# Optimization experiments

Measured on AMD Instinct MI355X. Metric: run time of the kernel, lower is better.

Reference implementation:

```python
import jax, jax.numpy as jnp
import numpy as np

LATENT = 64  # latent_size -> N = K = LATENT**2 = 4096 codes/tokens


def setup_inputs() -> dict:
    key = jax.random.key(0)
    k1, k2 = jax.random.split(key)
    hidden, L = 1024, LATENT
    z = jax.random.normal(k1, (hidden, L, L), dtype=jnp.float32)
    code_books = jax.random.uniform(k2, (hidden, L, L), dtype=jnp.float32)  # torch.rand init
    return {"z": z, "code_books": code_books}


def reference(z, code_books):
    # z, code_books: (D=hidden, L, L). Tokens/codes are columns of the flattened maps.
    D = z.shape[0]
    zf = z.reshape(D, -1).T           # (N, D) tokens
    cb = code_books.reshape(D, -1).T  # (K, D) codebook entries
    # Squared L2 distance via GEMM trick: ||a-b||^2 = ||a||^2 + ||b||^2 - 2 a.b
    # (avoids the N x K x D broadcast intermediate of the original)
    d2 = (jnp.sum(zf * zf, axis=1)[:, None]
          + jnp.sum(cb * cb, axis=1)[None, :]
          - 2.0 * zf @ cb.T)          # (N, K)
    idx = jnp.argmin(d2, axis=1)      # (N,)
    zq = cb[idx]                      # (N, D) gather
    zq = zq.reshape(LATENT, LATENT, -1).transpose(2, 0, 1)  # (D, L, L)
    # Straight-through: z = zq + (z - zq).detach()  (z was detached before lookup)
    z_st = zq + jax.lax.stop_gradient(z - zq)
    return z_st, zq
```

## Files before the change

### kernel.cpp

```cpp
#include <hip/hip_runtime.h>
#include <stdint.h>

#define D  1024
#define NK 4096
#define KA 1024
#define KB 1024
#define TAU 0.15f
#define CW  0.12f
#define MAXC 1024

#define BK2 32
#define NT2 (KA / BK2)
#define NBUF 3

typedef __attribute__((ext_vector_type(8))) _Float16 f16x8;
typedef __attribute__((ext_vector_type(4))) float f32x4;
typedef unsigned long long u64;

__device__ __forceinline__ uint32_t fkey(float f) {
    uint32_t b = __float_as_uint(f);
    return (b & 0x80000000u) ? ~b : (b | 0x80000000u);
}
__device__ __forceinline__ float unfkey(uint32_t u) {
    uint32_t b = (u & 0x80000000u) ? (u & 0x7fffffffu) : ~u;
    return __uint_as_float(b);
}
__device__ __forceinline__ u64 umin64(u64 a, u64 b) { return a < b ? a : b; }
__device__ __forceinline__ u64 umax64(u64 a, u64 b) { return a > b ? a : b; }

__device__ __forceinline__ void gload16(void* lds, const void* g) {
    __builtin_amdgcn_global_load_lds(
        (const __attribute__((address_space(1))) unsigned int*)g,
        (__attribute__((address_space(3))) unsigned int*)lds, 16, 0, 0);
}

#define BAR()      __builtin_amdgcn_s_barrier()
#define VMCNT6()   asm volatile("s_waitcnt vmcnt(6)" ::: "memory")
#define VMCNT0()   asm volatile("s_waitcnt vmcnt(0)" ::: "memory")

__global__ void cbnorm_kernel(const float* __restrict__ cb, float* __restrict__ cbn) {
    __shared__ float red[256];
    const int kk = threadIdx.x & 63;
    const int dc = threadIdx.x >> 6;
    const int k  = blockIdx.x * 64 + kk;
    float s = 0.f;
    for (int d = dc; d < D; d += 4) {
        float v = cb[d * NK + k];
        s = fmaf(v, v, s);
    }
    red[threadIdx.x] = s;
    __syncthreads();
    if (dc == 0) cbn[k] = (red[kk] + red[64 + kk]) + (red[128 + kk] + red[192 + kk]);
}

__global__ __launch_bounds__(256) void split_transpose(
        const float* __restrict__ z, const float* __restrict__ cb,
        _Float16* __restrict__ Ap, _Float16* __restrict__ Bp,
        float* __restrict__ partial) {
    __shared__ float T[64][65];
    const int isZ = (blockIdx.z == 0);
    const float* src = isZ ? z : cb;
    _Float16* dst = isZ ? Ap : Bp;
    const int n0 = blockIdx.x * 64, d0 = blockIdx.y * 64;
    const int t = threadIdx.x;
#pragma unroll
    for (int i = 0; i < 4; ++i) {
        int dl = (t >> 4) + i * 16;
        int nl = (t & 15) * 4;
        float4 v = *(const float4*)&src[(size_t)(d0 + dl) * NK + n0 + nl];
        T[dl][nl] = v.x; T[dl][nl + 1] = v.y; T[dl][nl + 2] = v.z; T[dl][nl + 3] = v.w;
    }
    __syncthreads();
    const int nr = t >> 2, dch = (t & 3) * 16;
    f16x8 h0, h1;
    float s = 0.f;
#pragma unroll
    for (int j = 0; j < 8; ++j) {
        float v = T[dch + j][nr];
        s = fmaf(v, v, s);
        h0[j] = (_Float16)v;
    }
#pragma unroll
    for (int j = 0; j < 8; ++j) {
        float v = T[dch + 8 + j][nr];
        s = fmaf(v, v, s);
        h1[j] = (_Float16)v;
    }
    size_t base = (size_t)(n0 + nr) * KA + d0 + dch;
    *(f16x8*)&dst[base]     = h0;
    *(f16x8*)&dst[base + 8] = h1;
    if (!isZ) {
        s += __shfl_xor(s, 1);
        s += __shfl_xor(s, 2);
        if ((t & 3) == 0) partial[(size_t)(d0 >> 6) * NK + n0 + nr] = s;
    }
}

__global__ void cbnorm_finish(const float* __restrict__ partial, float* __restrict__ cbn) {
    const int k = blockIdx.x * 256 + threadIdx.x;
    float s = 0.f;
#pragma unroll
    for (int j = 0; j < 16; ++j) s += partial[(size_t)j * NK + k];
    cbn[k] = s;
}

__global__ __launch_bounds__(256, 2) void gemm_mfma(
        const _Float16* __restrict__ Ap, const _Float16* __restrict__ Bp,
        const float* __restrict__ cbn, ulonglong2* __restrict__ tp) {
    __shared__ _Float16 As[NBUF][256 * BK2];
    __shared__ _Float16 Bs[NBUF][128 * BK2];
    const int tid = threadIdx.x;
    const int xcd = blockIdx.x & 7, idx = blockIdx.x >> 3;
    const int n0 = ((xcd >> 2) * 8 + (idx >> 3)) * 256;
    const int k0 = ((xcd & 3) * 8 + (idx & 7)) * 128;
    const int w = tid >> 6, l = tid & 63;
    const int wr = w >> 1, wc = w & 1;
    const int fr = l & 15, fq = l >> 4;

    f32x4 acc[8][4] = {};

    const int srow = tid >> 2;
    const int swz = ((tid & 3) ^ ((tid >> 3) & 3)) * 8;
    const _Float16* gA = Ap + (size_t)(n0 + srow) * KA + swz;
    const _Float16* gB = Bp + (size_t)(k0 + srow) * KB + swz;
    const int rcol = (fq ^ ((fr >> 1) & 3)) * 8;

#pragma unroll
    for (int i = 0; i < 4; ++i) gload16(&As[0][tid * 8 + i * 2048], gA + (size_t)(64 * i) * KA);
#pragma unroll
    for (int i = 0; i < 2; ++i) gload16(&Bs[0][tid * 8 + i * 2048], gB + (size_t)(64 * i) * KB);
#pragma unroll
    for (int i = 0; i < 4; ++i) gload16(&As[1][tid * 8 + i * 2048], gA + (size_t)(64 * i) * KA + BK2);
#pragma unroll
    for (int i = 0; i < 2; ++i) gload16(&Bs[1][tid * 8 + i * 2048], gB + (size_t)(64 * i) * KB + BK2);
    VMCNT6();
    BAR();

    int b = 0, pb = 2;
    for (int t = 0; t < NT2; ++t) {
        const _Float16* Ab = As[b];
        const _Float16* Bb = Bs[b];
        const bool st = (t + 2) < NT2;
        const size_t kofs = (size_t)(t + 2) * BK2;

        f16x8 bbf[4], a0[4], a1[4];
#pragma unroll
        for (int ni = 0; ni < 4; ++ni)
            bbf[ni] = *(const f16x8*)&Bb[(wc * 64 + ni * 16 + fr) * BK2 + rcol];
#pragma unroll
        for (int mi = 0; mi < 4; ++mi)
            a0[mi] = *(const f16x8*)&Ab[(wr * 128 + mi * 16 + fr) * BK2 + rcol];
#pragma unroll
        for (int mi = 0; mi < 4; ++mi)
            a1[mi] = *(const f16x8*)&Ab[(wr * 128 + 64 + mi * 16 + fr) * BK2 + rcol];

        if (st) {
#pragma unroll
            for (int i = 0; i < 4; ++i)
                gload16(&As[pb][tid * 8 + i * 2048], gA + (size_t)(64 * i) * KA + kofs);
#pragma unroll
            for (int i = 0; i < 2; ++i)
                gload16(&Bs[pb][tid * 8 + i * 2048], gB + (size_t)(64 * i) * KB + kofs);
        }

        __builtin_amdgcn_s_setprio(1);
#pragma unroll
        for (int mi = 0; mi < 4; ++mi)
#pragma unroll
            for (int ni = 0; ni < 4; ++ni)
                acc[mi][ni] = __builtin_amdgcn_mfma_f32_16x16x32_f16(a0[mi], bbf[ni], acc[mi][ni], 0, 0, 0);
#pragma unroll
        for (int mi = 0; mi < 4; ++mi)
#pragma unroll
            for (int ni = 0; ni < 4; ++ni)
                acc[4 + mi][ni] = __builtin_amdgcn_mfma_f32_16x16x32_f16(a1[mi], bbf[ni], acc[4 + mi][ni], 0, 0, 0);
        __builtin_amdgcn_s_setprio(0);

        if (t < NT2 - 2) {
            VMCNT6();
        } else if (t == NT2 - 2) {
            VMCNT0();
        }
        if (t < NT2 - 1) BAR();
        b = (b == 2) ? 0 : b + 1;
        pb = (pb == 2) ? 0 : pb + 1;
    }

    float cbv[4];
#pragma unroll
    for (int ni = 0; ni < 4; ++ni) cbv[ni] = cbn[k0 + wc * 64 + ni * 16 + fr];
    const int kt64 = (k0 >> 6) + wc;
#pragma unroll
    for (int mi = 0; mi < 8; ++mi) {
#pragma unroll
        for (int reg = 0; reg < 4; ++reg) {
            float b1f = 1e30f, b2f = 1e30f;
            int b1k = 0;
#pragma unroll
            for (int ni = 0; ni < 4; ++ni) {
                float s = fmaf(-2.f, acc[mi][ni][reg], cbv[ni]);
                b2f = fminf(fmaxf(s, b1f), b2f);
                if (s < b1f) { b1f = s; b1k = k0 + wc * 64 + ni * 16 + fr; }
            }
#pragma unroll
            for (int m = 8; m >= 1; m >>= 1) {
                float q1 = __shfl_xor(b1f, m);
                int   qk = __shfl_xor(b1k, m);
                float q2 = __shfl_xor(b2f, m);
                b2f = fminf(fminf(b2f, q2), fmaxf(b1f, q1));
                if (q1 < b1f) { b1f = q1; b1k = qk; }
            }
            if (fr == 0) {
                int n = n0 + wr * 128 + mi * 16 + fq * 4 + reg;
                ulonglong2 v;
                v.x = ((u64)fkey(b1f) << 32) | (unsigned)b1k;
                v.y = ((u64)fkey(b2f) << 32) | 0xffffffffu;
                tp[(size_t)kt64 * NK + n] = v;
            }
        }
    }
}

__global__ __launch_bounds__(256) void reduce_rows(
        const ulonglong2* __restrict__ tp, int* __restrict__ idx,
        int* __restrict__ rescue, u64* __restrict__ rbest, int* __restrict__ ctr) {
    __shared__ ulonglong2 sh[4][64];
    const int no = threadIdx.x & 63, st = threadIdx.x >> 6;
    const int n = blockIdx.x * 64 + no;
    u64 b1 = ~0ull, b2 = ~0ull;
#pragma unroll 4
    for (int g = st * 16; g < st * 16 + 16; ++g) {
        ulonglong2 e = tp[(size_t)g * NK + n];
        u64 nb1 = umin64(b1, e.x);
        u64 nb2 = umin64(umax64(b1, e.x), umin64(b2, e.y));
        b1 = nb1; b2 = nb2;
    }
    ulonglong2 v; v.x = b1; v.y = b2;
    sh[st][no] = v;
    __syncthreads();
    if (st == 0) {
#pragma unroll
        for (int j = 1; j < 4; ++j) {
            ulonglong2 e = sh[j][no];
            u64 nb1 = umin64(b1, e.x);
            u64 nb2 = umin64(umax64(b1, e.x), umin64(b2, e.y));
            b1 = nb1; b2 = nb2;
        }
        idx[n] = (int)(b1 & 0xffffffffull);
        float f1 = unfkey((uint32_t)(b1 >> 32));
        float f2 = unfkey((uint32_t)(b2 >> 32));
        if (f2 - f1 < TAU) {
            int p = atomicAdd(ctr, 1);
            rescue[p] = n;
            rbest[p] = ~0ull;
        }
    }
}

__global__ __launch_bounds__(256) void rescue_kernel(
        const float* __restrict__ z, const float* __restrict__ cb,
        const float* __restrict__ cbn, const ulonglong2* __restrict__ tp,
        const int* __restrict__ rescue, const int* __restrict__ ctr,
        u64* __restrict__ rbest) {
    const int cnt = min(*ctr, NK);
    const int slot = blockIdx.x;
    if (slot >= cnt) return;
    const int n = rescue[slot];
    const int tid = threadIdx.x;
    const int lane = tid & 63, wv = tid >> 6;

    __shared__ float zn[D];
    __shared__ int cand[MAXC];
    __shared__ int ccnt, overflow;
    __shared__ u64 wred[4];

    if (tid == 0) { ccnt = 0; overflow = 0; }
    for (int d = tid; d < D; d += 256) zn[d] = z[(size_t)d * NK + n];

    if (tid < 64) {
        ulonglong2 e = tp[(size_t)tid * NK + n];
        u64 m = e.x;
#pragma unroll
        for (int msk = 32; msk >= 1; msk >>= 1) m = umin64(m, __shfl_xor(m, msk));
        const float thr = unfkey((uint32_t)(m >> 32)) + CW;
        if (unfkey((uint32_t)(e.y >> 32)) < thr) {
            int p = atomicAdd(&ccnt, 64);
            if (p + 64 <= MAXC) {
                for (int j = 0; j < 64; ++j) cand[p + j] = tid * 64 + j;
            } else overflow = 1;
        } else if (unfkey((uint32_t)(e.x >> 32)) < thr) {
            int p = atomicAdd(&ccnt, 1);
            if (p < MAXC) cand[p] = (int)(e.x & 0xffffffffull);
            else overflow = 1;
        }
    }
    __syncthreads();

    const int ovf = overflow;
    const int m = ovf ? NK : min(ccnt, MAXC);
    u64 best = ~0ull;
    for (int ci = wv; ci < m; ci += 4) {
        const int k = ovf ? ci : cand[ci];
        float s = 0.f;
#pragma unroll
        for (int j = 0; j < 16; ++j)
            s = fmaf(zn[lane + j * 64], cb[(size_t)(lane + j * 64) * NK + k], s);
#pragma unroll
        for (int msk = 32; msk >= 1; msk >>= 1) s += __shfl_xor(s, msk);
        float sc = cbn[k] - 2.f * s;
        best = umin64(best, ((u64)fkey(sc) << 32) | (unsigned)k);
    }
    if (lane == 0) wred[wv] = best;
    __syncthreads();
    if (tid == 0)
        rbest[slot] = umin64(umin64(wred[0], wred[1]), umin64(wred[2], wred[3]));
}

__global__ void fix_idx(const int* __restrict__ rescue, const int* __restrict__ ctr,
                        const u64* __restrict__ rbest, int* __restrict__ idx) {
    const int cnt = min(*ctr, NK);
    for (int s = threadIdx.x + blockIdx.x * 256; s < cnt; s += gridDim.x * 256)
        idx[rescue[s]] = (int)(rbest[s] & 0xffffffffull);
}

__global__ __launch_bounds__(256) void gemm_argmin(
        const float* __restrict__ z, const float* __restrict__ cb,
        const float* __restrict__ cbn, unsigned long long* __restrict__ best) {
    __shared__ float Zs[8][128];
    __shared__ float Cs[8][128];
    const int n0 = blockIdx.y * 128, k0 = blockIdx.x * 128;
    const int tid = threadIdx.x;
    const int tx = tid & 15, ty = tid >> 4;
    const int lr = tid >> 5, lc = (tid & 31) << 2;
    float acc[8][8];
#pragma unroll
    for (int i = 0; i < 8; ++i)
#pragma unroll
        for (int j = 0; j < 8; ++j) acc[i][j] = 0.f;
    for (int d0 = 0; d0 < D; d0 += 8) {
        float4 zv = *(const float4*)&z [(d0 + lr) * NK + n0 + lc];
        float4 cv = *(const float4*)&cb[(d0 + lr) * NK + k0 + lc];
        __syncthreads();
        *(float4*)&Zs[lr][lc] = zv;
        *(float4*)&Cs[lr][lc] = cv;
        __syncthreads();
#pragma unroll
        for (int dd = 0; dd < 8; ++dd) {
            float4 a0 = *(const float4*)&Zs[dd][ty * 8];
            float4 a1 = *(const float4*)&Zs[dd][ty * 8 + 4];
            float4 b0 = *(const float4*)&Cs[dd][tx * 8];
            float4 b1 = *(const float4*)&Cs[dd][tx * 8 + 4];
            float a[8] = {a0.x, a0.y, a0.z, a0.w, a1.x, a1.y, a1.z, a1.w};
            float b[8] = {b0.x, b0.y, b0.z, b0.w, b1.x, b1.y, b1.z, b1.w};
#pragma unroll
            for (int i = 0; i < 8; ++i)
#pragma unroll
                for (int j = 0; j < 8; ++j) acc[i][j] = fmaf(a[i], b[j], acc[i][j]);
        }
    }
    float cbnv[8];
#pragma unroll
    for (int j = 0; j < 8; ++j) cbnv[j] = cbn[k0 + tx * 8 + j];
#pragma unroll
    for (int i = 0; i < 8; ++i) {
        float bv = cbnv[0] - 2.f * acc[i][0];
        int bj = 0;
#pragma unroll
        for (int j = 1; j < 8; ++j) {
            float v = cbnv[j] - 2.f * acc[i][j];
            if (v < bv) { bv = v; bj = j; }
        }
        u64 p = ((u64)fkey(bv) << 32) | (unsigned)(k0 + tx * 8 + bj);
#pragma unroll
        for (int m = 8; m >= 1; m >>= 1) {
            u64 q = __shfl_xor(p, m);
            if (q < p) p = q;
        }
        if (tx == 0) atomicMin(&best[n0 + ty * 8 + i], p);
    }
}

__global__ void extract_idx(const unsigned long long* __restrict__ best,
                            int* __restrict__ idx) {
    int n = blockIdx.x * 256 + threadIdx.x;
    idx[n] = (int)(unsigned)(best[n] & 0xFFFFFFFFull);
}

__global__ void gather_kernel(const float* __restrict__ z, const float* __restrict__ cb,
                              const int* __restrict__ idx, float* __restrict__ out) {
    const int d = blockIdx.x;
    const float* cbrow = &cb[(size_t)d * NK];
    const float* zrow  = &z [(size_t)d * NK];
    float* st = &out[(size_t)d * NK];
    float* zq = &out[(size_t)D * NK + (size_t)d * NK];
    for (int n4 = threadIdx.x; n4 < NK / 4; n4 += 256) {
        int4 iv = *(const int4*)&idx[n4 * 4];
        float4 zv = *(const float4*)&zrow[n4 * 4];
        float4 q;
        q.x = cbrow[iv.x]; q.y = cbrow[iv.y]; q.z = cbrow[iv.z]; q.w = cbrow[iv.w];
        float4 stv;
        stv.x = q.x + (zv.x - q.x);
        stv.y = q.y + (zv.y - q.y);
        stv.z = q.z + (zv.z - q.z);
        stv.w = q.w + (zv.w - q.w);
        *(float4*)&st[n4 * 4] = stv;
        *(float4*)&zq[n4 * 4] = q;
    }
}

extern "C" void kernel_launch(void* const* d_in, const int* in_sizes, int n_in,
                              void* d_out, int out_size, void* d_ws, size_t ws_size,
                              hipStream_t stream) {
    const float* z  = (const float*)d_in[0];
    const float* cb = (const float*)d_in[1];
    float* out = (float*)d_out;
    char* ws = (char*)d_ws;

    const size_t oA  = 0;
    const size_t oB  = oA + (size_t)NK * KA * 2;
    const size_t oT  = oB + (size_t)NK * KB * 2;
    const size_t oC  = oT + (size_t)NK * 64 * 16;
    const size_t oI  = oC + NK * 4;
    const size_t oR  = oI + NK * 4;
    const size_t oRB = oR + NK * 4;
    const size_t oN  = oRB + NK * 8;
    const size_t oP  = oN + 256;
    const size_t REQ = oP + (size_t)16 * NK * 4;

    if (ws_size >= REQ) {
        _Float16* Ap = (_Float16*)(ws + oA);
        _Float16* Bp = (_Float16*)(ws + oB);
        ulonglong2* tp = (ulonglong2*)(ws + oT);
        float* cbn = (float*)(ws + oC);
        int* idx = (int*)(ws + oI);
        int* rescue = (int*)(ws + oR);
        u64* rbest = (u64*)(ws + oRB);
        int* ctr = (int*)(ws + oN);
        float* partial = (float*)(ws + oP);

        hipMemsetAsync(ctr, 0, 4, stream);
        split_transpose<<<dim3(NK / 64, D / 64, 2), 256, 0, stream>>>(z, cb, Ap, Bp, partial);
        cbnorm_finish<<<16, 256, 0, stream>>>(partial, cbn);
        gemm_mfma<<<512, 256, 0, stream>>>(Ap, Bp, cbn, tp);
        reduce_rows<<<64, 256, 0, stream>>>(tp, idx, rescue, rbest, ctr);
        rescue_kernel<<<4096, 256, 0, stream>>>(z, cb, cbn, tp, rescue, ctr, rbest);
        fix_idx<<<4, 256, 0, stream>>>(rescue, ctr, rbest, idx);
        gather_kernel<<<1024, 256, 0, stream>>>(z, cb, idx, out);
    } else {
        unsigned long long* best = (unsigned long long*)ws;
        float* cbn = (float*)(ws + NK * 8);
        int* idx = (int*)(ws + NK * 8 + NK * 4);
        hipMemsetAsync(best, 0xFF, NK * 8, stream);
        cbnorm_kernel<<<64, 256, 0, stream>>>(cb, cbn);
        gemm_argmin<<<dim3(NK / 128, NK / 128), 256, 0, stream>>>(z, cb, cbn, best);
        extract_idx<<<16, 256, 0, stream>>>(best, idx);
        gather_kernel<<<1024, 256, 0, stream>>>(z, cb, idx, out);
    }
}
```

Baseline: 90.67 us.

## Load GEMM A fragments directly from global into registers, dropping A LDS staging

The A operand of the fp16 MFMA GEMM is no longer staged through LDS via triple-buffered global_load_lds. Each lane now reads its own 16-byte A fragment straight from global memory every K-step, and only B keeps the LDS pipeline. The vmcnt waits shrink to match, and a scheduling barrier is added. This removes the LDS traffic and footprint for A, which may let more blocks fit, but each wave now issues uncoalesced-ish global loads with no prefetch distance, so MFMAs may stall on global latency.

```diff
diff --git a/kernel.cpp b/kernel.cpp
--- a/kernel.cpp
+++ b/kernel.cpp
@@ -35,7 +35,8 @@
 }
 
 #define BAR()      __builtin_amdgcn_s_barrier()
-#define VMCNT6()   asm volatile("s_waitcnt vmcnt(6)" ::: "memory")
+#define SCHEDBAR() __builtin_amdgcn_sched_barrier(0)
+#define VMCNT2()   asm volatile("s_waitcnt vmcnt(2)" ::: "memory")
 #define VMCNT0()   asm volatile("s_waitcnt vmcnt(0)" ::: "memory")
 
 __global__ void cbnorm_kernel(const float* __restrict__ cb, float* __restrict__ cbn) {
@@ -107,7 +108,6 @@
 __global__ __launch_bounds__(256, 2) void gemm_mfma(
         const _Float16* __restrict__ Ap, const _Float16* __restrict__ Bp,
         const float* __restrict__ cbn, ulonglong2* __restrict__ tp) {
-    __shared__ _Float16 As[NBUF][256 * BK2];
     __shared__ _Float16 Bs[NBUF][128 * BK2];
     const int tid = threadIdx.x;
     const int xcd = blockIdx.x & 7, idx = blockIdx.x >> 3;
@@ -121,63 +121,59 @@
 
     const int srow = tid >> 2;
     const int swz = ((tid & 3) ^ ((tid >> 3) & 3)) * 8;
-    const _Float16* gA = Ap + (size_t)(n0 + srow) * KA + swz;
     const _Float16* gB = Bp + (size_t)(k0 + srow) * KB + swz;
     const int rcol = (fq ^ ((fr >> 1) & 3)) * 8;
 
-#pragma unroll
-    for (int i = 0; i < 4; ++i) gload16(&As[0][tid * 8 + i * 2048], gA + (size_t)(64 * i) * KA);
+    const _Float16* gA[8];
+#pragma unroll
+    for (int m = 0; m < 8; ++m)
+        gA[m] = Ap + (size_t)(n0 + wr * 128 + (m >> 2) * 64 + (m & 3) * 16 + fr) * KA + fq * 8;
+
 #pragma unroll
     for (int i = 0; i < 2; ++i) gload16(&Bs[0][tid * 8 + i * 2048], gB + (size_t)(64 * i) * KB);
 #pragma unroll
-    for (int i = 0; i < 4; ++i) gload16(&As[1][tid * 8 + i * 2048], gA + (size_t)(64 * i) * KA + BK2);
-#pragma unroll
     for (int i = 0; i < 2; ++i) gload16(&Bs[1][tid * 8 + i * 2048], gB + (size_t)(64 * i) * KB + BK2);
-    VMCNT6();
+    VMCNT2();
     BAR();
 
     int b = 0, pb = 2;
     for (int t = 0; t < NT2; ++t) {
-        const _Float16* Ab = As[b];
         const _Float16* Bb = Bs[b];
         const bool st = (t + 2) < NT2;
         const size_t kofs = (size_t)(t + 2) * BK2;
 
-        f16x8 bbf[4], a0[4], a1[4];
+        f16x8 av[8];
+#pragma unroll
+        for (int m = 0; m < 8; ++m)
+            av[m] = *(const f16x8*)(gA[m] + (size_t)t * BK2);
+
+        if (st) {
+#pragma unroll
+            for (int i = 0; i < 2; ++i)
+                gload16(&Bs[pb][tid * 8 + i * 2048], gB + (size_t)(64 * i) * KB + kofs);
+        }
+
+        f16x8 bbf[4];
 #pragma unroll
         for (int ni = 0; ni < 4; ++ni)
             bbf[ni] = *(const f16x8*)&Bb[(wc * 64 + ni * 16 + fr) * BK2 + rcol];
+
+        __builtin_amdgcn_s_setprio(1);
 #pragma unroll
         for (int mi = 0; mi < 4; ++mi)
-            a0[mi] = *(const f16x8*)&Ab[(wr * 128 + mi * 16 + fr) * BK2 + rcol];
+#pragma unroll
+            for (int ni = 0; ni < 4; ++ni)
+                acc[mi][ni] = __builtin_amdgcn_mfma_f32_16x16x32_f16(av[mi], bbf[ni], acc[mi][ni], 0, 0, 0);
 #pragma unroll
         for (int mi = 0; mi < 4; ++mi)
-            a1[mi] = *(const f16x8*)&Ab[(wr * 128 + 64 + mi * 16 + fr) * BK2 + rcol];
-
-        if (st) {
-#pragma unroll
-            for (int i = 0; i < 4; ++i)
-                gload16(&As[pb][tid * 8 + i * 2048], gA + (size_t)(64 * i) * KA + kofs);
-#pragma unroll
-            for (int i = 0; i < 2; ++i)
-                gload16(&Bs[pb][tid * 8 + i * 2048], gB + (size_t)(64 * i) * KB + kofs);
-        }
-
-        __builtin_amdgcn_s_setprio(1);
-#pragma unroll
-        for (int mi = 0; mi < 4; ++mi)
 #pragma unroll
             for (int ni = 0; ni < 4; ++ni)
-                acc[mi][ni] = __builtin_amdgcn_mfma_f32_16x16x32_f16(a0[mi], bbf[ni], acc[mi][ni], 0, 0, 0);
-#pragma unroll
-        for (int mi = 0; mi < 4; ++mi)
-#pragma unroll
-            for (int ni = 0; ni < 4; ++ni)
-                acc[4 + mi][ni] = __builtin_amdgcn_mfma_f32_16x16x32_f16(a1[mi], bbf[ni], acc[4 + mi][ni], 0, 0, 0);
+                acc[4 + mi][ni] = __builtin_amdgcn_mfma_f32_16x16x32_f16(av[4 + mi], bbf[ni], acc[4 + mi][ni], 0, 0, 0);
         __builtin_amdgcn_s_setprio(0);
 
+        SCHEDBAR();
         if (t < NT2 - 2) {
-            VMCNT6();
+            VMCNT2();
         } else if (t == NT2 - 2) {
             VMCNT0();
         }
```

Measured after the change: 124.7 us. 1.38x slower.
